# Optimization experiments

Hardware: AMD Instinct MI355X
Metric: run time of the kernel (lower is better)

The kernel has to match this reference:

```python
import jax, jax.numpy as jnp
import numpy as np

T, B, D, N, REL, OUT = 16, 128, 96, 8, 96, 64  # time, batch, slot_size, num_slot, rel_size, out_att_size
EPS = 1e-5


def setup_inputs() -> dict:
    key = jax.random.key(0)
    ks = jax.random.split(key, 12)
    rn = lambda k, shape, s: jax.random.normal(k, shape, dtype=jnp.float32) * s
    stdev_i = 1.0 / np.sqrt(2.0 * D)
    stdev_r = 1.0 / np.sqrt(2.0 * D + N)
    return {
        'x': jax.random.normal(ks[0], (T, B, D), dtype=jnp.float32),
        'Wqkv': rn(ks[1], (D, 3 * N), 0.1), 'bqkv': jnp.zeros((3 * N,), jnp.float32),
        'ln_g': jnp.ones((D, 3 * N), jnp.float32), 'ln_b': jnp.zeros((D, 3 * N), jnp.float32),
        'a1': rn(ks[2], (), 0.1), 'a2': rn(ks[3], (), 0.1), 'a3': rn(ks[4], (), 0.1),
        'W2': rn(ks[5], (N * D, D), 0.03), 'b2': jnp.zeros((D,), jnp.float32),
        'Wr': rn(ks[6], (D * D, REL), 0.01), 'br': jnp.zeros((REL,), jnp.float32),
        'W3': rn(ks[7], (N * REL, OUT), 0.03), 'b3': jnp.zeros((OUT,), jnp.float32),
        'item_bias': jax.random.uniform(ks[8], (D, D), jnp.float32, -stdev_i, stdev_i),
        'rel_bias': jax.random.uniform(ks[9], (N, D, D), jnp.float32, -stdev_r, stdev_r),
    }


def reference(x, Wqkv, bqkv, ln_g, ln_b, a1, a2, a3, W2, b2, Wr, br, W3, b3, item_bias, rel_bias):
    Bb = x.shape[1]
    Mi0 = jnp.broadcast_to(item_bias, (Bb, D, D))
    rel0 = jnp.broadcast_to(rel_bias, (Bb, N, D, D))
    W2r = W2.reshape(N, D, D)  # rel_projector2 weight, rows indexed by flattened (n, d)

    def step(carry, xt):  # xt: [B, D]
        Mi, rel = carry
        Mi = Mi + xt[:, :, None] * xt[:, None, :]                     # Mi + outer(x, x)
        Vtr = jnp.einsum('bdf,bndf->bf', Mi, rel)                     # [B, D]
        X2 = Vtr[:, :, None] * xt[:, None, :]                         # [B, D, D]
        qkv = (Mi + a2 * X2) @ Wqkv + bqkv                            # [B, D, 3N]
        mu = qkv.mean(axis=(1, 2), keepdims=True)                     # LayerNorm over [D, 3N]
        var = qkv.var(axis=(1, 2), keepdims=True)
        qkv = (qkv - mu) * jax.lax.rsqrt(var + EPS) * ln_g + ln_b
        qkv = qkv.transpose(0, 2, 1)                                  # [B, 3N, D]
        q, k, v = qkv[:, :N], qkv[:, N:2 * N], qkv[:, 2 * N:]
        # op_att: out[b,i] = sum_j outer(tanh(q_i * k_j), v_j)
        t = jnp.tanh(q[:, :, None, :] * k[:, None, :, :])             # [B, N, N, D]
        R0 = jnp.einsum('bijd,bje->bide', t, v)                       # [B, N, D, D]
        rel = a1 * rel + R0
        R2 = jnp.einsum('bnde,ndf->bef', R0, W2r) + b2                # [B, D, D]
        Mi = Mi + a3 * R2
        r_vec = (rel.reshape(Bb, N, D * D) @ Wr + br).reshape(Bb, N * REL)
        out = r_vec @ W3 + b3                                          # [B, OUT]
        return (Mi, rel), out

    (_, _), hx = jax.lax.scan(step, (Mi0, rel0), x)
    return hx  # [T, B, OUT]
```

## Files before the change

### kernel.cpp

```cpp
#include <hip/hip_runtime.h>
#include <math.h>

#define T_ 16
#define B_ 128
#define C3 24
#define OUT_ 64
#define EPS_ 1e-5f

typedef __attribute__((ext_vector_type(8))) short bf16x8;
typedef __attribute__((ext_vector_type(4))) float f32x4;

union FragU { unsigned u[4]; bf16x8 f; };

__device__ __forceinline__ short f2bf(float x) {
    unsigned u = __float_as_uint(x);
    return (short)((u + 0x7fffu + ((u >> 16) & 1u)) >> 16);
}
__device__ __forceinline__ void splitf(float x, short& h, short& l) {
    unsigned u = __float_as_uint(x);
    unsigned hb = (u + 0x7fffu + ((u >> 16) & 1u)) & 0xffff0000u;
    float res = x - __uint_as_float(hb);
    unsigned v = __float_as_uint(res);
    h = (short)(hb >> 16);
    l = (short)((v + 0x7fffu + ((v >> 16) & 1u)) >> 16);
}
__device__ __forceinline__ f32x4 mfma16(bf16x8 a, bf16x8 b, f32x4 c) {
    return __builtin_amdgcn_mfma_f32_16x16x32_bf16(a, b, c, 0, 0, 0);
}
__device__ __forceinline__ f32x4 mfma16v(bf16x8 a, bf16x8 b, f32x4 c) {
    f32x4 d;
    asm("s_nop 1\n\tv_mfma_f32_16x16x32_bf16 %0, %1, %2, %3"
        : "=v"(d)
        : "v"(a), "v"(b), "0"(c));
    return d;
}
#define MFMA_FENCE4(a0, a1, a2, a3) \
    asm volatile("s_nop 7\n\ts_nop 7" : "+v"(a0), "+v"(a1), "+v"(a2), "+v"(a3))

__device__ __forceinline__ float fast_tanh(float z) {
    float a = fminf(fabsf(z), 9.0f);
    float e = __expf(2.0f * a);
    float t = 1.0f - 2.0f / (e + 1.0f);
    return copysignf(t, z);
}

__global__ __launch_bounds__(768, 1) void prep_mega(
    const float* __restrict__ Wr, const float* __restrict__ W2, const float* __restrict__ W3,
    const float* __restrict__ rel_bias,
    short* __restrict__ WrBH, short* __restrict__ WrBL,
    short* __restrict__ W2H, short* __restrict__ W2L,
    short* __restrict__ W3H, short* __restrict__ W3L,
    float* __restrict__ y0)
{
    const int bid = blockIdx.x, tid = threadIdx.x;
    if (bid < 1152) {
        int idx = bid * 768 + tid;
        int jj = idx & 7, lane = (idx >> 3) & 63, f = idx >> 9;
        int kf = f % 3, rt = (f / 3) % 6, d = f / 18;
        int col = lane & 15, grp = lane >> 4;
        int e = kf * 32 + grp * 8 + jj;
        int r = rt * 16 + col;
        short h, l; splitf(Wr[(size_t)(d * 96 + e) * 96 + r], h, l);
        WrBH[idx] = h; WrBL[idx] = l;
    } else if (bid < 1248) {
        int idx = (bid - 1152) * 768 + tid;
        int jj = idx & 7, lane = (idx >> 3) & 63, kb = (idx >> 9) % 24, rt = idx / (512 * 24);
        int col = lane & 15, grp = lane >> 4;
        int kp = kb * 32 + grp * 8 + jj;
        int d = kp >> 3, n = kp & 7;
        int f = rt * 16 + col;
        short h, l; splitf(W2[(size_t)(n * 96 + d) * 96 + f], h, l);
        W2H[idx] = h; W2L[idx] = l;
    } else if (bid < 1312) {
        int idx = (bid - 1248) * 768 + tid;
        int jj = idx & 7, lane = (idx >> 3) & 63, kb = (idx >> 9) % 24, ot = idx / (512 * 24);
        int col = lane & 15, grp = lane >> 4;
        int k = kb * 32 + grp * 8 + jj, o = ot * 16 + col;
        short h, l; splitf(W3[(size_t)k * 64 + o], h, l);
        W3H[idx] = h; W3L[idx] = l;
    } else {
        __shared__ float s[768];
        const int blk = bid - 1312;
        const int n = blk >> 3, sl = blk & 7;
        const int r = tid % 96, p = tid / 96;
        const float* rb = rel_bias + n * 9216 + sl * 1152;
        float acc = 0.f;
        for (int i = p * 144; i < p * 144 + 144; ++i)
            acc += rb[i] * Wr[(size_t)(sl * 1152 + i) * 96 + r];
        s[tid] = acc;
        __syncthreads();
        if (tid < 96) {
            float tot = 0.f;
            for (int q = 0; q < 8; ++q) tot += s[q * 96 + tid];
            atomicAdd(&y0[n * 96 + tid], tot);
        }
    }
}

__global__ __attribute__((amdgpu_flat_work_group_size(768, 768), amdgpu_waves_per_eu(3, 3)))
void stm_rec(
    const float* __restrict__ x, const float* __restrict__ Wqkv, const float* __restrict__ bqkv,
    const float* __restrict__ ln_g, const float* __restrict__ ln_b,
    const float* __restrict__ a1p, const float* __restrict__ a2p, const float* __restrict__ a3p,
    const float* __restrict__ b2,
    const float* __restrict__ item_bias, const float* __restrict__ rel_bias,
    const short* __restrict__ W2H, const short* __restrict__ W2L,
    short* __restrict__ t2g, short* __restrict__ vgb)
{
    __shared__ __attribute__((aligned(16))) char smem[102336];
    const int tid = threadIdx.x;
    const int b = blockIdx.x;
    const int wv = tid >> 6, lane = tid & 63, col = lane & 15, grp = lane >> 4;
    const float a1 = a1p[0], a2 = a2p[0], a3 = a3p[0];

    float* s_xall    = (float*)(smem);
    float* s_scr     = (float*)(smem + 6144);
    float* s_scrB    = (float*)(smem + 15360);
    float* s_Wq      = (float*)(smem + 18432);
    float* s_lng     = (float*)(smem + 27648);
    float* s_lnb     = (float*)(smem + 36864);
    float* s_tsum    = (float*)(smem + 46080);
    float* s_v       = (float*)(smem + 49152);
    float* s_G0      = (float*)(smem + 52224);
    float* s_G1      = (float*)(smem + 55296);
    float* s_xtWqAll = (float*)(smem + 58368);
    float* s_b2Wq    = (float*)(smem + 59904);
    float* s_bq      = (float*)(smem + 60000);
    float* s_b2v     = (float*)(smem + 60096);
    float* s_red     = (float*)(smem + 60480);
    short* s_tH      = (short*)(smem + 60608);
    short* s_tL      = (short*)(smem + 73024);
    short* s_t2L     = (short*)(smem + 85440);
    float* s_vp      = (float*)(smem + 97728);

    const int de = tid >> 3, ef0 = (tid & 7) * 12;
    float rMi[12], rS[12], rQ[3];
#pragma unroll
    for (int ii = 0; ii < 12; ++ii) {
        int idx = de * 96 + ef0 + ii;
        rMi[ii] = item_bias[idx];
        float ss = 0.f;
        for (int n = 0; n < 8; ++n) ss += rel_bias[n * 9216 + idx];
        rS[ii] = ss;
    }

    for (int i = tid; i < 1536; i += 768)
        s_xall[i] = x[((size_t)(i / 96) * B_ + b) * 96 + (i % 96)];
    for (int i = tid; i < 2304; i += 768) {
        s_Wq[i] = Wqkv[i]; s_lng[i] = ln_g[i]; s_lnb[i] = ln_b[i];
    }
    if (tid < 24) s_bq[tid] = bqkv[tid];
    if (tid < 96) s_b2v[tid] = b2[tid];
    __syncthreads();
#pragma unroll
    for (int pp = 0; pp < 3; ++pp) {
        int o = tid + 768 * pp; int i = o / C3, c = o % C3;
        float acc = 0.f;
        const float* ib = item_bias + i * 96;
        for (int k = 0; k < 96; ++k) acc += ib[k] * s_Wq[k * C3 + c];
        rQ[pp] = acc;
    }
    { int c = tid % C3, p = tid / C3; float acc = 0.f;
      for (int k = 3 * p; k < 3 * p + 3; ++k) acc += s_b2v[k] * s_Wq[k * C3 + c];
      s_scr[tid] = acc; }
    if (tid < 384) {
        int t = tid / 24, c = tid % 24;
        float acc = 0.f;
        const float* xr = s_xall + t * 96;
        for (int k = 0; k < 96; ++k) acc += xr[k] * s_Wq[k * C3 + c];
        s_xtWqAll[tid] = acc;
    }
    __syncthreads();
    if (tid < C3) { float a = 0.f; for (int p = 0; p < 32; ++p) a += s_scr[p * C3 + tid]; s_b2Wq[tid] = a; }
    __syncthreads();

    for (int t = 0; t < T_; ++t) {
        const float* xt = s_xall + t * 96;
        const float* xtWq = s_xtWqAll + t * 24;
        {
            float xde = xt[de];
            const float4* xp = (const float4*)&xt[ef0];
            float4 x0 = xp[0], x1 = xp[1], x2 = xp[2];
            rMi[0] += xde * x0.x; rMi[1] += xde * x0.y; rMi[2] += xde * x0.z; rMi[3] += xde * x0.w;
            rMi[4] += xde * x1.x; rMi[5] += xde * x1.y; rMi[6] += xde * x1.z; rMi[7] += xde * x1.w;
            rMi[8] += xde * x2.x; rMi[9] += xde * x2.y; rMi[10] += xde * x2.z; rMi[11] += xde * x2.w;
        }
        {
            float p12[12];
#pragma unroll
            for (int ii = 0; ii < 12; ++ii) p12[ii] = rMi[ii] * rS[ii];
#pragma unroll
            for (int ii = 0; ii < 12; ++ii) {
                p12[ii] += __shfl_xor(p12[ii], 8);
                p12[ii] += __shfl_xor(p12[ii], 16);
                p12[ii] += __shfl_xor(p12[ii], 32);
            }
            if ((lane >> 3) == 0) {
#pragma unroll
                for (int ii = 0; ii < 12; ++ii)
                    s_vp[wv * 96 + (lane & 7) * 12 + ii] = p12[ii];
            }
        }
        __syncthreads();
        {
            const int i0 = tid / 24, c = tid % 24;
            float ls = 0.f, lq = 0.f;
#pragma unroll
            for (int pp = 0; pp < 3; ++pp) {
                const int i = i0 + 32 * pp;
                float vtr = 0.f;
#pragma unroll
                for (int w = 0; w < 12; ++w) vtr += s_vp[w * 96 + i];
                rQ[pp] += xt[i] * xtWq[c];
                float qv = rQ[pp] + a2 * vtr * xtWq[c] + s_bq[c];
                s_scr[tid + 768 * pp] = qv;
                ls += qv; lq += qv * qv;
            }
            for (int off = 32; off > 0; off >>= 1) { ls += __shfl_down(ls, off); lq += __shfl_down(lq, off); }
            if (lane == 0) { s_red[wv] = ls; s_red[16 + wv] = lq; }
        }
        __syncthreads();
        {
            float S = 0.f, Qs = 0.f;
            for (int w = 0; w < 12; ++w) { S += s_red[w]; Qs += s_red[16 + w]; }
            const float mu = S * (1.0f / 2304.f);
            const float rstd = rsqrtf(Qs * (1.0f / 2304.f) - mu * mu + EPS_);
            const int j = tid / 96, d = tid % 96;
            {
                int o = d * C3 + 16 + j;
                float vv = (s_scr[o] - mu) * rstd * s_lng[o] + s_lnb[o];
                s_v[tid] = vv;
                vgb[((size_t)(t * B_ + b)) * 768 + tid] = f2bf(vv);
            }
            int ok = d * C3 + 8 + j;
            float kk = (s_scr[ok] - mu) * rstd * s_lng[ok] + s_lnb[ok];
            float tv0, tv1;
            unsigned hp0, hp1, hp2, hp3, lp0, lp1, lp2, lp3;
            float ts = 0.f;
#pragma unroll
            for (int q = 0; q < 4; ++q) {
                int oq0 = d * C3 + 2 * q, oq1 = oq0 + 1;
                float q0 = (s_scr[oq0] - mu) * rstd * s_lng[oq0] + s_lnb[oq0];
                float q1 = (s_scr[oq1] - mu) * rstd * s_lng[oq1] + s_lnb[oq1];
                tv0 = fast_tanh(q0 * kk);
                tv1 = fast_tanh(q1 * kk);
                ts += tv0 + tv1;
                short h0, l0, h1, l1;
                splitf(tv0, h0, l0); splitf(tv1, h1, l1);
                unsigned hh = (unsigned)(unsigned short)h0 | ((unsigned)(unsigned short)h1 << 16);
                unsigned ll = (unsigned)(unsigned short)l0 | ((unsigned)(unsigned short)l1 << 16);
                if (q == 0) { hp0 = hh; lp0 = ll; }
                else if (q == 1) { hp1 = hh; lp1 = ll; }
                else if (q == 2) { hp2 = hh; lp2 = ll; }
                else { hp3 = hh; lp3 = ll; }
                s_t2L[(2 * q) * 768 + d * 8 + j] = h0;
                s_t2L[(2 * q + 1) * 768 + d * 8 + j] = h1;
            }
            *(uint4*)&s_tH[j * 776 + d * 8] = make_uint4(hp0, hp1, hp2, hp3);
            *(uint4*)&s_tL[j * 776 + d * 8] = make_uint4(lp0, lp1, lp2, lp3);
            s_tsum[j * 96 + d] = ts;
        }
        __syncthreads();
        *(uint4*)&t2g[((size_t)(t * B_ + b)) * 6144 + tid * 8] = *(const uint4*)&s_t2L[tid * 8];
        {
            const int rt = wv % 6, kh = wv / 6;
            f32x4 aHH = {0,0,0,0}, aLH = {0,0,0,0}, aHL = {0,0,0,0}, aLL = {0,0,0,0};
#pragma unroll 4
            for (int s2 = 0; s2 < 12; ++s2) {
                int kb = kh * 12 + s2;
                bf16x8 ah = {}; bf16x8 al = {};
                if (col < 8) {
                    ah = *(const bf16x8*)&s_tH[col * 776 + kb * 32 + grp * 8];
                    al = *(const bf16x8*)&s_tL[col * 776 + kb * 32 + grp * 8];
                }
                int fo = ((rt * 24 + kb) * 64 + lane) * 8;
                bf16x8 bh = *(const bf16x8*)&W2H[fo];
                bf16x8 bl = *(const bf16x8*)&W2L[fo];
                aHH = mfma16v(ah, bh, aHH);
                aLH = mfma16v(al, bh, aLH);
                aHL = mfma16v(ah, bl, aHL);
                aLL = mfma16v(al, bl, aLL);
            }
            MFMA_FENCE4(aHH, aLH, aHL, aLL);
            f32x4 accG;
#pragma unroll
            for (int reg = 0; reg < 4; ++reg) accG[reg] = (aHH[reg] + aLH[reg]) + (aHL[reg] + aLL[reg]);
            float* dst = (kh == 0) ? s_G0 : s_G1;
            if (grp < 2) {
#pragma unroll
                for (int reg = 0; reg < 4; ++reg)
                    dst[(grp * 4 + reg) * 96 + rt * 16 + col] = accG[reg];
            }
        }
        __syncthreads();
        { int oo = tid % 192, q = tid / 192; int jg = oo / C3, cc = oo % C3;
          float a = 0.f;
          for (int f = q * 24; f < q * 24 + 24; ++f)
              a += (s_G0[jg * 96 + f] + s_G1[jg * 96 + f]) * s_Wq[f * C3 + cc];
          s_scrB[tid] = a; }
        {
            float sn[12], r2[12];
#pragma unroll
            for (int ii = 0; ii < 12; ++ii) { sn[ii] = 0.f; r2[ii] = 0.f; }
#pragma unroll
            for (int j = 0; j < 8; ++j) {
                const float tj = s_tsum[j * 96 + de];
                const float vj = s_v[j * 96 + de];
                const float4* vp = (const float4*)&s_v[j * 96 + ef0];
                const float4* g0 = (const float4*)&s_G0[j * 96 + ef0];
                const float4* g1 = (const float4*)&s_G1[j * 96 + ef0];
#pragma unroll
                for (int q4 = 0; q4 < 3; ++q4) {
                    float4 vv = vp[q4], ga = g0[q4], gb = g1[q4];
                    float gx = ga.x + gb.x, gy = ga.y + gb.y, gz = ga.z + gb.z, gw = ga.w + gb.w;
                    sn[q4*4+0] += tj*vv.x; sn[q4*4+1] += tj*vv.y;
                    sn[q4*4+2] += tj*vv.z; sn[q4*4+3] += tj*vv.w;
                    r2[q4*4+0] += vj*gx; r2[q4*4+1] += vj*gy;
                    r2[q4*4+2] += vj*gz; r2[q4*4+3] += vj*gw;
                }
            }
#pragma unroll
            for (int ii = 0; ii < 12; ++ii) {
                rS[ii] = a1 * rS[ii] + sn[ii];
                rMi[ii] += a3 * (r2[ii] + s_b2v[ef0 + ii]);
            }
        }
        __syncthreads();
#pragma unroll
        for (int pp = 0; pp < 3; ++pp) {
            int o = tid + 768 * pp; int i = o / C3, c = o % C3;
            float a = s_b2Wq[c];
#pragma unroll
            for (int j = 0; j < 8; ++j) {
                float g = s_scrB[j * C3 + c] + s_scrB[192 + j * C3 + c]
                        + s_scrB[384 + j * C3 + c] + s_scrB[576 + j * C3 + c];
                a += s_v[j * 96 + i] * g;
            }
            rQ[pp] += a3 * a;
        }
    }
}

__global__ __launch_bounds__(384, 2) void stm_tail(
    const short* __restrict__ WrBH, const short* __restrict__ WrBL,
    const short* __restrict__ W3H, const short* __restrict__ W3L,
    const short* __restrict__ t2g, const short* __restrict__ vgb,
    const float* __restrict__ y0, const float* __restrict__ br,
    const float* __restrict__ W3f, const float* __restrict__ b3,
    float* __restrict__ zg, float* __restrict__ c0v, float* __restrict__ cbrv)
{
    __shared__ __attribute__((aligned(16))) short sPT[6 * 5120];
    short* DyH = sPT;
    short* DyL = sPT + 6208;

    const int tid = threadIdx.x;

    if (blockIdx.x >= 256) {
        float* red = (float*)sPT;
        const int o = tid & 63, seg = tid >> 6;
        if (blockIdx.x == 256) {
            float pa = 0.f;
            for (int i = seg * 128; i < seg * 128 + 128; ++i)
                pa += y0[i] * W3f[(size_t)i * 64 + o];
            red[seg * 64 + o] = pa;
            __syncthreads();
            if (tid < 64) {
                float s = 0.f;
                for (int q = 0; q < 6; ++q) s += red[q * 64 + tid];
                c0v[tid] = s;
            }
        } else {
            float pb = 0.f;
            for (int i = seg * 128; i < seg * 128 + 128; ++i)
                pb += br[i % 96] * W3f[(size_t)i * 64 + o];
            red[seg * 64 + o] = pb;
            __syncthreads();
            if (tid < 64) {
                float s = b3[tid];
                for (int q = 0; q < 6; ++q) s += red[q * 64 + tid];
                cbrv[tid] = s;
            }
        }
        return;
    }

    const int b = blockIdx.x & 127, tg = blockIdx.x >> 7;
    const int wv6 = tid >> 6, lane = tid & 63, col = lane & 15, grp = lane >> 4;
    const int rt6 = wv6;
    const int th = tg * 8;
    short* PTw = sPT + wv6 * 5120;

    bf16x8 Av[4][3];
#pragma unroll
    for (int p = 0; p < 4; ++p)
#pragma unroll
        for (int kf = 0; kf < 3; ++kf) {
            int t = th + 2 * p + (col >> 3);
            int j = col & 7;
            uint4 z = *(const uint4*)&vgb[((size_t)(t * B_ + b)) * 768 + j * 96 + kf * 32 + grp * 8];
            FragU F; F.u[0] = z.x; F.u[1] = z.y; F.u[2] = z.z; F.u[3] = z.w;
            Av[p][kf] = F.f;
        }
    f32x4 accD[8];
#pragma unroll
    for (int btl = 0; btl < 8; ++btl) accD[btl] = (f32x4){0.f, 0.f, 0.f, 0.f};

    FragU A2r[8];
    bf16x8 bhA[3], blA[3], bhB[3], blB[3];
#pragma unroll
    for (int kf = 0; kf < 3; ++kf) {
        const int fo = ((0 * 18 + rt6 * 3 + kf) * 64 + lane) * 8;
        bhA[kf] = *(const bf16x8*)&WrBH[fo];
        blA[kf] = *(const bf16x8*)&WrBL[fo];
    }

#define TAIL_BODY(DL, CH, CL, NH, NL)                                          \
    {                                                                          \
        const int d = g4 * 4 + (DL);                                           \
        if ((DL) < 3 || g4 < 23) {                                             \
            const int dn = d + 1;                                              \
            _Pragma("unroll")                                                  \
            for (int kf = 0; kf < 3; ++kf) {                                   \
                const int fo = ((dn * 18 + rt6 * 3 + kf) * 64 + lane) * 8;     \
                NH[kf] = *(const bf16x8*)&WrBH[fo];                            \
                NL[kf] = *(const bf16x8*)&WrBL[fo];                            \
            }                                                                  \
        }                                                                      \
        if ((DL) == 1) {                                                       \
            _Pragma("unroll")                                                  \
            for (int btl = 0; btl < 8; ++btl) {                                \
                A2r[btl].u[0] = 0; A2r[btl].u[1] = 0;                          \
                A2r[btl].u[2] = 0; A2r[btl].u[3] = 0;                          \
                if (col < 8) {                                                 \
                    const int tt = th + btl;                                   \
                    uint4 z = *(const uint4*)&t2g[((size_t)(tt * B_ + b)) * 6144 \
                              + col * 768 + g4 * 32 + grp * 8];                \
                    A2r[btl].u[0] = z.x; A2r[btl].u[1] = z.y;                  \
                    A2r[btl].u[2] = z.z; A2r[btl].u[3] = z.w;                  \
                }                                                              \
            }                                                                  \
        }                                                                      \
        f32x4 aPv[4];                                                          \
        _Pragma("unroll")                                                      \
        for (int p = 0; p < 4; ++p) aPv[p] = (f32x4){0.f, 0.f, 0.f, 0.f};      \
        _Pragma("unroll")                                                      \
        for (int kf = 0; kf < 3; ++kf) {                                       \
            _Pragma("unroll")                                                  \
            for (int p = 0; p < 4; ++p) aPv[p] = mfma16(Av[p][kf], CH[kf], aPv[p]); \
            _Pragma("unroll")                                                  \
            for (int p = 0; p < 4; ++p) aPv[p] = mfma16(Av[p][kf], CL[kf], aPv[p]); \
        }                                                                      \
        {                                                                      \
            const int j0 = (grp & 1) * 4;                                      \
            const int bo = grp >> 1;                                           \
            _Pragma("unroll")                                                  \
            for (int p = 0; p < 4; ++p) {                                      \
                const int btl = 2 * p + bo;                                    \
                uint2 uu;                                                      \
                uu.x = (unsigned)(unsigned short)f2bf(aPv[p][0]) |             \
                       ((unsigned)(unsigned short)f2bf(aPv[p][1]) << 16);      \
                uu.y = (unsigned)(unsigned short)f2bf(aPv[p][2]) |             \
                       ((unsigned)(unsigned short)f2bf(aPv[p][3]) << 16);      \
                *(uint2*)&PTw[btl * 640 + col * 40 + (DL) * 8 + j0] = uu;      \
            }                                                                  \
        }                                                                      \
        if ((DL) == 3) {                                                       \
            _Pragma("unroll")                                                  \
            for (int btl = 0; btl < 8; ++btl) {                                \
                bf16x8 B2 = *(const bf16x8*)&PTw[btl * 640 + col * 40 + grp * 8]; \
                accD[btl] = mfma16(A2r[btl].f, B2, accD[btl]);                 \
            }                                                                  \
        }                                                                      \
    }

    for (int g4 = 0; g4 < 24; ++g4) {
        TAIL_BODY(0, bhA, blA, bhB, blB)
        TAIL_BODY(1, bhB, blB, bhA, blA)
        TAIL_BODY(2, bhA, blA, bhB, blB)
        TAIL_BODY(3, bhB, blB, bhA, blA)
    }
#undef TAIL_BODY

    __syncthreads();
    if (grp < 2) {
#pragma unroll
        for (int btl = 0; btl < 8; ++btl)
#pragma unroll
            for (int reg = 0; reg < 4; ++reg) {
                short h, l; splitf(accD[btl][reg], h, l);
                int idx = btl * 776 + (grp * 4 + reg) * 96 + rt6 * 16 + col;
                DyH[idx] = h; DyL[idx] = l;
            }
    }
    __syncthreads();
    if (wv6 < 4) {
        const int ot = wv6;
        f32x4 zHH = {0,0,0,0}, zLH = {0,0,0,0}, zHL = {0,0,0,0};
#pragma unroll 4
        for (int kb = 0; kb < 24; ++kb) {
            bf16x8 ah = {}; bf16x8 al = {};
            if (col < 8) {
                ah = *(const bf16x8*)&DyH[col * 776 + kb * 32 + grp * 8];
                al = *(const bf16x8*)&DyL[col * 776 + kb * 32 + grp * 8];
            }
            int fo = ((ot * 24 + kb) * 64 + lane) * 8;
            bf16x8 bhw = *(const bf16x8*)&W3H[fo];
            bf16x8 blw = *(const bf16x8*)&W3L[fo];
            zHH = mfma16(ah, bhw, zHH);
            zLH = mfma16(al, bhw, zLH);
            zHL = mfma16(ah, blw, zHL);
        }
        if (grp < 2) {
#pragma unroll
            for (int reg = 0; reg < 4; ++reg) {
                int tl = grp * 4 + reg;
                zg[((size_t)(b * 16 + th + tl)) * 64 + ot * 16 + col] = zHH[reg] + zLH[reg] + zHL[reg];
            }
        }
    }
}

__global__ __launch_bounds__(64) void stm_fin(
    const float* __restrict__ a1p, const float* __restrict__ zg,
    const float* __restrict__ c0v, const float* __restrict__ cbrv,
    float* __restrict__ out)
{
    const int tid = threadIdx.x, b = blockIdx.x;
    const float a1 = a1p[0];
    float u = c0v[tid];
    const float cbr = cbrv[tid];
    for (int t = 0; t < T_; ++t) {
        u = a1 * u + zg[((size_t)(b * 16 + t)) * 64 + tid];
        out[((size_t)(t * B_ + b)) * OUT_ + tid] = u + cbr;
    }
}

extern "C" void kernel_launch(void* const* d_in, const int* in_sizes, int n_in,
                              void* d_out, int out_size, void* d_ws, size_t ws_size,
                              hipStream_t stream) {
    const float* x         = (const float*)d_in[0];
    const float* Wqkv      = (const float*)d_in[1];
    const float* bqkv      = (const float*)d_in[2];
    const float* ln_g      = (const float*)d_in[3];
    const float* ln_b      = (const float*)d_in[4];
    const float* a1        = (const float*)d_in[5];
    const float* a2        = (const float*)d_in[6];
    const float* a3        = (const float*)d_in[7];
    const float* W2        = (const float*)d_in[8];
    const float* b2        = (const float*)d_in[9];
    const float* Wr        = (const float*)d_in[10];
    const float* br        = (const float*)d_in[11];
    const float* W3        = (const float*)d_in[12];
    const float* b3        = (const float*)d_in[13];
    const float* item_bias = (const float*)d_in[14];
    const float* rel_bias  = (const float*)d_in[15];
    float* out = (float*)d_out;

    char* ws = (char*)d_ws;
    short* WrBH = (short*)ws;
    short* WrBL = (short*)(ws + 1769472);
    short* W2H  = (short*)(ws + 3538944);
    short* W2L  = (short*)(ws + 3686400);
    short* W3H  = (short*)(ws + 3833856);
    short* W3L  = (short*)(ws + 3932160);
    float* y0   = (float*)(ws + 4030464);
    short* t2g  = (short*)(ws + 4034048);
    short* vgb  = (short*)(ws + 29199872);
    float* zg   = (float*)(ws + 32345600);
    float* c0v  = (float*)(ws + 32869888);
    float* cbrv = (float*)(ws + 32870144);

    hipMemsetAsync(y0, 0, 3072, stream);
    hipLaunchKernelGGL(prep_mega, dim3(1376), dim3(768), 0, stream,
                       Wr, W2, W3, rel_bias, WrBH, WrBL, W2H, W2L, W3H, W3L, y0);
    hipLaunchKernelGGL(stm_rec, dim3(B_), dim3(768), 0, stream,
                       x, Wqkv, bqkv, ln_g, ln_b, a1, a2, a3,
                       b2, item_bias, rel_bias, W2H, W2L, t2g, vgb);
    hipLaunchKernelGGL(stm_tail, dim3(258), dim3(384), 0, stream,
                       WrBH, WrBL, W3H, W3L, t2g, vgb,
                       y0, br, W3, b3, zg, c0v, cbrv);
    hipLaunchKernelGGL(stm_fin, dim3(B_), dim3(64), 0, stream,
                       a1, zg, c0v, cbrv, out);
}
```

Baseline: 493.5 us.

## Move per-thread rS state from registers to LDS and pad LN buffers

Moves the 12-element per-thread relation sum rS out of registers into shared memory with a stride of 13, to ease register pressure under the 3-waves-per-EU bound. It also pads the qkv scratch and LayerNorm gamma/beta arrays from row stride 24 to 25 to reduce LDS bank conflicts. The sn and r2 accumulation loops are split so fewer accumulators are live at once. The cost is more LDS traffic each step and a larger shared allocation (about 140 KB), which may limit occupancy.

```diff
diff --git a/kernel.cpp b/kernel.cpp
--- a/kernel.cpp
+++ b/kernel.cpp
@@ -107,7 +107,7 @@
     const short* __restrict__ W2H, const short* __restrict__ W2L,
     short* __restrict__ t2g, short* __restrict__ vgb)
 {
-    __shared__ __attribute__((aligned(16))) char smem[102336];
+    __shared__ __attribute__((aligned(16))) char smem[143424];
     const int tid = threadIdx.x;
     const int b = blockIdx.x;
     const int wv = tid >> 6, lane = tid & 63, col = lane & 15, grp = lane >> 4;
@@ -115,39 +115,44 @@
 
     float* s_xall    = (float*)(smem);
     float* s_scr     = (float*)(smem + 6144);
-    float* s_scrB    = (float*)(smem + 15360);
-    float* s_Wq      = (float*)(smem + 18432);
-    float* s_lng     = (float*)(smem + 27648);
-    float* s_lnb     = (float*)(smem + 36864);
-    float* s_tsum    = (float*)(smem + 46080);
-    float* s_v       = (float*)(smem + 49152);
-    float* s_G0      = (float*)(smem + 52224);
-    float* s_G1      = (float*)(smem + 55296);
-    float* s_xtWqAll = (float*)(smem + 58368);
-    float* s_b2Wq    = (float*)(smem + 59904);
-    float* s_bq      = (float*)(smem + 60000);
-    float* s_b2v     = (float*)(smem + 60096);
-    float* s_red     = (float*)(smem + 60480);
-    short* s_tH      = (short*)(smem + 60608);
-    short* s_tL      = (short*)(smem + 73024);
-    short* s_t2L     = (short*)(smem + 85440);
-    float* s_vp      = (float*)(smem + 97728);
+    float* s_scrB    = (float*)(smem + 15744);
+    float* s_Wq      = (float*)(smem + 18816);
+    float* s_lng     = (float*)(smem + 28032);
+    float* s_lnb     = (float*)(smem + 37632);
+    float* s_tsum    = (float*)(smem + 47232);
+    float* s_v       = (float*)(smem + 50304);
+    float* s_G0      = (float*)(smem + 53376);
+    float* s_G1      = (float*)(smem + 56448);
+    float* s_xtWqAll = (float*)(smem + 59520);
+    float* s_b2Wq    = (float*)(smem + 61056);
+    float* s_bq      = (float*)(smem + 61152);
+    float* s_b2v     = (float*)(smem + 61248);
+    float* s_red     = (float*)(smem + 61632);
+    short* s_tH      = (short*)(smem + 61760);
+    short* s_tL      = (short*)(smem + 74176);
+    short* s_t2L     = (short*)(smem + 86592);
+    float* s_vp      = (float*)(smem + 98880);
+    float* s_rS      = (float*)(smem + 103488);
 
     const int de = tid >> 3, ef0 = (tid & 7) * 12;
-    float rMi[12], rS[12], rQ[3];
+    const int t13 = tid * 13;
+    float rMi[12], rQ[3];
 #pragma unroll
     for (int ii = 0; ii < 12; ++ii) {
         int idx = de * 96 + ef0 + ii;
         rMi[ii] = item_bias[idx];
         float ss = 0.f;
         for (int n = 0; n < 8; ++n) ss += rel_bias[n * 9216 + idx];
-        rS[ii] = ss;
+        s_rS[t13 + ii] = ss;
     }
 
     for (int i = tid; i < 1536; i += 768)
         s_xall[i] = x[((size_t)(i / 96) * B_ + b) * 96 + (i % 96)];
     for (int i = tid; i < 2304; i += 768) {
-        s_Wq[i] = Wqkv[i]; s_lng[i] = ln_g[i]; s_lnb[i] = ln_b[i];
+        int dd = i / 24, cc = i % 24;
+        s_Wq[i] = Wqkv[i];
+        s_lng[dd * 25 + cc] = ln_g[i];
+        s_lnb[dd * 25 + cc] = ln_b[i];
     }
     if (tid < 24) s_bq[tid] = bqkv[tid];
     if (tid < 96) s_b2v[tid] = b2[tid];
@@ -162,7 +167,7 @@
     }
     { int c = tid % C3, p = tid / C3; float acc = 0.f;
       for (int k = 3 * p; k < 3 * p + 3; ++k) acc += s_b2v[k] * s_Wq[k * C3 + c];
-      s_scr[tid] = acc; }
+      s_scr[p * 25 + c] = acc; }
     if (tid < 384) {
         int t = tid / 24, c = tid % 24;
         float acc = 0.f;
@@ -171,7 +176,7 @@
         s_xtWqAll[tid] = acc;
     }
     __syncthreads();
-    if (tid < C3) { float a = 0.f; for (int p = 0; p < 32; ++p) a += s_scr[p * C3 + tid]; s_b2Wq[tid] = a; }
+    if (tid < C3) { float a = 0.f; for (int p = 0; p < 32; ++p) a += s_scr[p * 25 + tid]; s_b2Wq[tid] = a; }
     __syncthreads();
 
     for (int t = 0; t < T_; ++t) {
@@ -188,7 +193,7 @@
         {
             float p12[12];
 #pragma unroll
-            for (int ii = 0; ii < 12; ++ii) p12[ii] = rMi[ii] * rS[ii];
+            for (int ii = 0; ii < 12; ++ii) p12[ii] = rMi[ii] * s_rS[t13 + ii];
 #pragma unroll
             for (int ii = 0; ii < 12; ++ii) {
                 p12[ii] += __shfl_xor(p12[ii], 8);
@@ -213,7 +218,7 @@
                 for (int w = 0; w < 12; ++w) vtr += s_vp[w * 96 + i];
                 rQ[pp] += xt[i] * xtWq[c];
                 float qv = rQ[pp] + a2 * vtr * xtWq[c] + s_bq[c];
-                s_scr[tid + 768 * pp] = qv;
+                s_scr[i * 25 + c] = qv;
                 ls += qv; lq += qv * qv;
             }
             for (int off = 32; off > 0; off >>= 1) { ls += __shfl_down(ls, off); lq += __shfl_down(lq, off); }
@@ -226,20 +231,21 @@
             const float mu = S * (1.0f / 2304.f);
             const float rstd = rsqrtf(Qs * (1.0f / 2304.f) - mu * mu + EPS_);
             const int j = tid / 96, d = tid % 96;
+            const int d25 = d * 25;
             {
-                int o = d * C3 + 16 + j;
+                int o = d25 + 16 + j;
                 float vv = (s_scr[o] - mu) * rstd * s_lng[o] + s_lnb[o];
                 s_v[tid] = vv;
                 vgb[((size_t)(t * B_ + b)) * 768 + tid] = f2bf(vv);
             }
-            int ok = d * C3 + 8 + j;
+            int ok = d25 + 8 + j;
             float kk = (s_scr[ok] - mu) * rstd * s_lng[ok] + s_lnb[ok];
             float tv0, tv1;
             unsigned hp0, hp1, hp2, hp3, lp0, lp1, lp2, lp3;
             float ts = 0.f;
 #pragma unroll
             for (int q = 0; q < 4; ++q) {
-                int oq0 = d * C3 + 2 * q, oq1 = oq0 + 1;
+                int oq0 = d25 + 2 * q, oq1 = oq0 + 1;
                 float q0 = (s_scr[oq0] - mu) * rstd * s_lng[oq0] + s_lnb[oq0];
                 float q1 = (s_scr[oq1] - mu) * rstd * s_lng[oq1] + s_lnb[oq1];
                 tv0 = fast_tanh(q0 * kk);
@@ -299,31 +305,43 @@
               a += (s_G0[jg * 96 + f] + s_G1[jg * 96 + f]) * s_Wq[f * C3 + cc];
           s_scrB[tid] = a; }
         {
-            float sn[12], r2[12];
-#pragma unroll
-            for (int ii = 0; ii < 12; ++ii) { sn[ii] = 0.f; r2[ii] = 0.f; }
+            float sn[12];
+#pragma unroll
+            for (int ii = 0; ii < 12; ++ii) sn[ii] = 0.f;
 #pragma unroll
             for (int j = 0; j < 8; ++j) {
                 const float tj = s_tsum[j * 96 + de];
+                const float4* vp = (const float4*)&s_v[j * 96 + ef0];
+#pragma unroll
+                for (int q4 = 0; q4 < 3; ++q4) {
+                    float4 vv = vp[q4];
+                    sn[q4*4+0] += tj*vv.x; sn[q4*4+1] += tj*vv.y;
+                    sn[q4*4+2] += tj*vv.z; sn[q4*4+3] += tj*vv.w;
+                }
+            }
+#pragma unroll
+            for (int ii = 0; ii < 12; ++ii)
+                s_rS[t13 + ii] = a1 * s_rS[t13 + ii] + sn[ii];
+        }
+        {
+            float r2[12];
+#pragma unroll
+            for (int ii = 0; ii < 12; ++ii) r2[ii] = 0.f;
+#pragma unroll
+            for (int j = 0; j < 8; ++j) {
                 const float vj = s_v[j * 96 + de];
-                const float4* vp = (const float4*)&s_v[j * 96 + ef0];
                 const float4* g0 = (const float4*)&s_G0[j * 96 + ef0];
                 const float4* g1 = (const float4*)&s_G1[j * 96 + ef0];
 #pragma unroll
                 for (int q4 = 0; q4 < 3; ++q4) {
-                    float4 vv = vp[q4], ga = g0[q4], gb = g1[q4];
-                    float gx = ga.x + gb.x, gy = ga.y + gb.y, gz = ga.z + gb.z, gw = ga.w + gb.w;
-                    sn[q4*4+0] += tj*vv.x; sn[q4*4+1] += tj*vv.y;
-                    sn[q4*4+2] += tj*vv.z; sn[q4*4+3] += tj*vv.w;
-                    r2[q4*4+0] += vj*gx; r2[q4*4+1] += vj*gy;
-                    r2[q4*4+2] += vj*gz; r2[q4*4+3] += vj*gw;
+                    float4 ga = g0[q4], gb = g1[q4];
+                    r2[q4*4+0] += vj*(ga.x+gb.x); r2[q4*4+1] += vj*(ga.y+gb.y);
+                    r2[q4*4+2] += vj*(ga.z+gb.z); r2[q4*4+3] += vj*(ga.w+gb.w);
                 }
             }
 #pragma unroll
-            for (int ii = 0; ii < 12; ++ii) {
-                rS[ii] = a1 * rS[ii] + sn[ii];
+            for (int ii = 0; ii < 12; ++ii)
                 rMi[ii] += a3 * (r2[ii] + s_b2v[ef0 + ii]);
-            }
         }
         __syncthreads();
 #pragma unroll
```

Result: faster. 465.2 us (-5.7%).
